# Kernel tuning notes

Measured on AMD Instinct MI355X. Metric: run time of the kernel, lower is better.

## Reference

```python
import jax, jax.numpy as jnp
import numpy as np

N_HEADS = 4
NUM_GROUPS = 32
EPS = 1e-6


def _nin(t, W, b):
    # 1x1 conv as dense over channel dim: [B,C,H,W] x [C,D] -> [B,D,H,W]
    return jnp.einsum('bchw,cd->bdhw', t, W) + b[None, :, None, None]


def setup_inputs() -> dict:
    key = jax.random.key(0)
    ks = jax.random.split(key, 12)
    B, C, H, W = 8, 256, 32, 32
    Tc = 512
    Cin = C + Tc  # 768
    x = jax.random.normal(ks[0], (B, C, H, W), dtype=jnp.float32)
    text_feat = jax.random.normal(ks[1], (B, Tc), dtype=jnp.float32)
    gn_gamma = jnp.ones((Cin,), dtype=jnp.float32)
    gn_beta = jnp.zeros((Cin,), dtype=jnp.float32)
    scale = 1.0 / np.sqrt(Cin)
    W0 = jax.random.normal(ks[2], (Cin, C), dtype=jnp.float32) * scale
    b0 = jnp.zeros((C,), dtype=jnp.float32)
    W1 = jax.random.normal(ks[3], (Cin, C), dtype=jnp.float32) * scale
    b1 = jnp.zeros((C,), dtype=jnp.float32)
    W2 = jax.random.normal(ks[4], (Cin, C), dtype=jnp.float32) * scale
    b2 = jnp.zeros((C,), dtype=jnp.float32)
    return {"x": x, "text_feat": text_feat, "gn_gamma": gn_gamma, "gn_beta": gn_beta,
            "W0": W0, "b0": b0, "W1": W1, "b1": b1, "W2": W2, "b2": b2}


def reference(x, text_feat, gn_gamma, gn_beta, W0, b0, W1, b1, W2, b2):
    B, C, H, W = x.shape
    # broadcast text features spatially and concat on channel dim
    tf = jnp.broadcast_to(text_feat[:, :, None, None], (B, text_feat.shape[1], H, W))
    h = jnp.concatenate([x, tf], axis=1)  # [B, C+Tc, H, W]
    Ctot = h.shape[1]
    # GroupNorm(32, Ctot), eps=1e-6
    hg = h.reshape(B, NUM_GROUPS, Ctot // NUM_GROUPS, H, W)
    mu = hg.mean(axis=(2, 3, 4), keepdims=True)
    var = hg.var(axis=(2, 3, 4), keepdims=True)
    hn = ((hg - mu) * jax.lax.rsqrt(var + EPS)).reshape(B, Ctot, H, W)
    hn = hn * gn_gamma[None, :, None, None] + gn_beta[None, :, None, None]
    q = _nin(hn, W0, b0)
    k = _nin(hn, W1, b1)
    v = _nin(hn, W2, b2)
    Ch = C // N_HEADS
    qh = q.reshape(B * N_HEADS, Ch, H, W)
    kh = k.reshape(B * N_HEADS, Ch, H, W)
    vh = v.reshape(B * N_HEADS, Ch, H, W)
    # full HW x HW attention scores, softmax over flattened key positions
    w = jnp.einsum('bchw,bcij->bhwij', qh, kh) * (Ch ** -0.5)
    w = jax.nn.softmax(w.reshape(B * N_HEADS, H, W, H * W), axis=-1)
    w = w.reshape(B * N_HEADS, H, W, H, W)
    ho = jnp.einsum('bhwij,bcij->bchw', w, vh).reshape(B, C, H, W)
    return x + ho
```

## Files before the change

### kernel.cpp

```cpp
#include <hip/hip_runtime.h>
#include <math.h>

#define BATCH 8
#define CX 256
#define TC 512
#define CIN 768
#define HW_TOT 1024
#define NH 4
#define CHD 64

typedef __attribute__((ext_vector_type(8))) short short8;
typedef __attribute__((ext_vector_type(4))) short s4v;
typedef __attribute__((ext_vector_type(4))) float floatx4;
typedef __attribute__((ext_vector_type(4))) int int4v;

#define QSCALE 0.18033688f

static __device__ __forceinline__ short f2bf(float f) {
    union { float f; unsigned u; } c; c.f = f;
    unsigned r = (c.u + 0x7fffu + ((c.u >> 16) & 1u)) >> 16;
    return (short)r;
}

static __device__ __forceinline__ int pack_trunc(float lo, float hi) {
    union { float f; unsigned u; } L, H;
    L.f = lo; H.f = hi;
    return (int)((H.u & 0xffff0000u) | (L.u >> 16));
}

__global__ __launch_bounds__(256)
void gn_kernel(const float* __restrict__ x, const float* __restrict__ tf,
               const float* __restrict__ gamma, const float* __restrict__ beta,
               float* __restrict__ scale, float* __restrict__ shift,
               float* __restrict__ tc) {
    const int b = blockIdx.x >> 5;
    const int g = blockIdx.x & 31;
    const int t = threadIdx.x;
    const int w = t >> 6, lane = t & 63;
    if (blockIdx.x < 24) tc[blockIdx.x * 256 + t] = 0.f;

    float s = 0.f, ss = 0.f;
    #pragma unroll
    for (int rr = 0; rr < 6; rr++) {
        const int row = w * 6 + rr;
        const int cg = g * 24 + row;
        if (cg < CX) {
            const float4* p = (const float4*)(x + ((size_t)b * CX + cg) * HW_TOT);
            #pragma unroll
            for (int i = 0; i < 4; i++) {
                float4 v = p[lane + 64 * i];
                s += v.x + v.y + v.z + v.w;
                ss += v.x * v.x + v.y * v.y + v.z * v.z + v.w * v.w;
            }
        } else {
            float v = tf[b * TC + cg - CX];
            s += 16.f * v;
            ss += 16.f * v * v;
        }
    }
    #pragma unroll
    for (int d = 1; d < 64; d <<= 1) {
        s += __shfl_xor(s, d);
        ss += __shfl_xor(ss, d);
    }
    __shared__ float rs_[4], rss_[4];
    if (lane == 0) { rs_[w] = s; rss_[w] = ss; }
    __syncthreads();
    const float S  = rs_[0] + rs_[1] + rs_[2] + rs_[3];
    const float SS = rss_[0] + rss_[1] + rss_[2] + rss_[3];
    const float inv_n = 1.f / (24 * 1024);
    const float mean = S * inv_n;
    const float var = SS * inv_n - mean * mean;
    const float r = rsqrtf(var + 1e-6f);
    if (t < 24) {
        int cg = g * 24 + t;
        float sc = gamma[cg] * r;
        scale[b * CIN + cg] = sc;
        shift[b * CIN + cg] = beta[cg] - mean * sc;
    }
}

__global__ __launch_bounds__(256)
void prep_kernel(const float* __restrict__ x, const float* __restrict__ tf,
                 const float* __restrict__ scale, const float* __restrict__ shift,
                 const float* __restrict__ W0, const float* __restrict__ W1,
                 const float* __restrict__ W2,
                 short* __restrict__ hnT, short* __restrict__ Wt,
                 float* __restrict__ tc) {
    __shared__ float hs[128];
    __shared__ float red[4][64];
    const int bx = blockIdx.x;
    const int t = threadIdx.x;
    if (bx < 256) {
        int id = (bx & 31) * 256 + t;
        int b = id >> 10;
        const float* xb = x + (size_t)b * CX * HW_TOT + (id & 1023);
        const float* scb = scale + b * CIN;
        const float* shb = shift + b * CIN;
        short* outp = hnT + (size_t)id * CX;
        int c0base = (bx >> 5) * 32;
        for (int c0 = c0base; c0 < c0base + 32; c0 += 8) {
            short8 o;
            #pragma unroll
            for (int i = 0; i < 8; i++) {
                float v = xb[(size_t)(c0 + i) * HW_TOT];
                o[i] = f2bf(v * scb[c0 + i] + shb[c0 + i]);
            }
            *(short8*)(outp + c0) = o;
        }
    } else if (bx < 268) {
        int m = bx - 256;
        int dg = (m % 3) * 256 + t;
        int which = dg >> 8, d = dg & 255;
        const float* Wm = (which == 0) ? W0 : (which == 1) ? W1 : W2;
        int c0base = (m / 3) * 64;
        for (int c0 = c0base; c0 < c0base + 64; c0 += 8) {
            short8 o;
            #pragma unroll
            for (int i = 0; i < 8; i++) o[i] = f2bf(Wm[(size_t)(c0 + i) * CX + d]);
            *(short8*)(Wt + (size_t)dg * CX + c0) = o;
        }
    } else {
        int m = bx - 268;
        int ks = m & 3;
        int b = (m >> 2) & 7, dt = m >> 5;
        int which = dt >> 2, d0 = (dt & 3) * 64;
        const float* Wm = (which == 0) ? W0 : (which == 1) ? W1 : W2;
        if (t < 128) {
            int c = ks * 128 + t;
            hs[t] = tf[b * TC + c] * scale[b * CIN + CX + c] + shift[b * CIN + CX + c];
        }
        __syncthreads();
        int td = t & 63, tq = t >> 6;
        float acc = 0.f;
        const float* wp = Wm + (size_t)(CX + ks * 128 + tq * 32) * CX + d0 + td;
        #pragma unroll 8
        for (int c = 0; c < 32; c++)
            acc = fmaf(hs[tq * 32 + c], wp[(size_t)c * CX], acc);
        red[tq][td] = acc;
        __syncthreads();
        if (t < 64)
            atomicAdd(&tc[b * CIN + which * CX + d0 + t],
                      red[0][t] + red[1][t] + red[2][t] + red[3][t]);
    }
}

__global__ __launch_bounds__(256, 2)
void qkv_gemm(const short* __restrict__ hnT, const short* __restrict__ Wt,
              const float* __restrict__ tc,
              const float* __restrict__ b0, const float* __restrict__ b1,
              const float* __restrict__ b2,
              short* __restrict__ qb, short* __restrict__ kb, short* __restrict__ vb) {
    const int hw0 = blockIdx.x * 64, dt = blockIdx.y, b = blockIdx.z;
    const int which = dt >> 2;
    const int col0 = (dt & 3) * 64;
    const int dg0 = which * 256 + col0;
    const bool OV = (which == 2);

    __shared__ short At[64 * 256];
    __shared__ short Bt[64 * 256];

    const int t = threadIdx.x;
    const int w = t >> 6, l = t & 63;
    const int wm = w >> 1, wn = w & 1;
    const int l15 = l & 15, q = l >> 4;
    const int srow = t >> 2;
    const int cbase = (t & 3) * 8;
    const int sw = srow & 7;

    const short* gA = hnT + (size_t)(b * HW_TOT + hw0 + srow) * CX + cbase * 8;
    const short* gB = Wt + (size_t)(dg0 + srow) * CX + cbase * 8;

    short8 ra[8], rb[8];
    #pragma unroll
    for (int i = 0; i < 8; i++) ra[i] = *(const short8*)(gA + i * 8);
    #pragma unroll
    for (int i = 0; i < 8; i++) rb[i] = *(const short8*)(gB + i * 8);
    short* wA = At + srow * 256;
    short* wB = Bt + srow * 256;
    #pragma unroll
    for (int i = 0; i < 8; i++) *(short8*)(wA + ((cbase + i) ^ sw) * 8) = ra[i];
    #pragma unroll
    for (int i = 0; i < 8; i++) *(short8*)(wB + ((cbase + i) ^ sw) * 8) = rb[i];
    __syncthreads();

    const short* aB = OV ? Bt : At;
    const short* bB = OV ? At : Bt;

    floatx4 acc[2][2] = {};
    __builtin_amdgcn_s_setprio(1);
    #pragma unroll
    for (int kc = 0; kc < 8; kc++) {
        short8 af[2], bf2[2];
        #pragma unroll
        for (int mt = 0; mt < 2; mt++) {
            const int r = wm * 32 + mt * 16 + l15;
            af[mt] = *(const short8*)(aB + r * 256 + ((kc * 4 + q) ^ (r & 7)) * 8);
        }
        #pragma unroll
        for (int nt = 0; nt < 2; nt++) {
            const int r = wn * 32 + nt * 16 + l15;
            bf2[nt] = *(const short8*)(bB + r * 256 + ((kc * 4 + q) ^ (r & 7)) * 8);
        }
        #pragma unroll
        for (int mt = 0; mt < 2; mt++)
            #pragma unroll
            for (int nt = 0; nt < 2; nt++)
                acc[mt][nt] = __builtin_amdgcn_mfma_f32_16x16x32_bf16(
                    af[mt], bf2[nt], acc[mt][nt], 0, 0, 0);
    }
    __builtin_amdgcn_s_setprio(0);

    __syncthreads();
    const float* bias = (which == 0) ? b0 : (which == 1) ? b1 : b2;
    if (!OV) {
        const float qs = (which == 0) ? QSCALE : 1.0f;
        float cadd[2];
        #pragma unroll
        for (int nt = 0; nt < 2; nt++) {
            int d = col0 + wn * 32 + nt * 16 + l15;
            cadd[nt] = bias[d] + tc[b * CIN + which * CX + d];
        }
        #pragma unroll
        for (int mt = 0; mt < 2; mt++)
            #pragma unroll
            for (int rr = 0; rr < 4; rr++)
                #pragma unroll
                for (int nt = 0; nt < 2; nt++)
                    At[(wm * 32 + mt * 16 + q * 4 + rr) * 72 + wn * 32 + nt * 16 + l15]
                        = f2bf((acc[mt][nt][rr] + cadd[nt]) * qs);
    } else {
        #pragma unroll
        for (int mt = 0; mt < 2; mt++)
            #pragma unroll
            for (int rr = 0; rr < 4; rr++) {
                int d = col0 + wm * 32 + mt * 16 + q * 4 + rr;
                float radd = bias[d] + tc[b * CIN + 2 * CX + d];
                #pragma unroll
                for (int nt = 0; nt < 2; nt++)
                    At[(wm * 32 + mt * 16 + q * 4 + rr) * 72 + wn * 32 + nt * 16 + l15]
                        = f2bf(acc[mt][nt][rr] + radd);
            }
    }
    __syncthreads();
    const int sch2 = (t & 3) * 16;
    short8 v0 = *(const short8*)(At + srow * 72 + sch2);
    short8 v1 = *(const short8*)(At + srow * 72 + sch2 + 8);
    if (!OV) {
        short* outp = (which == 0) ? qb : kb;
        size_t off = (size_t)(b * HW_TOT + hw0 + srow) * CX + col0 + sch2;
        *(short8*)(outp + off) = v0;
        *(short8*)(outp + off + 8) = v1;
    } else {
        size_t off = (size_t)(b * CX + col0 + srow) * HW_TOT + hw0 + sch2;
        *(short8*)(vb + off) = v0;
        *(short8*)(vb + off + 8) = v1;
    }
}

__global__ __launch_bounds__(256, 3)
void attn_kernel(const short* __restrict__ qb, const short* __restrict__ kb,
                 const short* __restrict__ vb, const float* __restrict__ x,
                 float* __restrict__ out) {
    const int qt = blockIdx.x, bh = blockIdx.y;
    const int b = bh >> 2, h = bh & 3;
    const int hw0 = qt * 64;

    __shared__ short Qs[64 * 72];
    __shared__ short Ks[2][64 * 72];
    __shared__ short Vs[2][64 * 72];

    const int t = threadIdx.x;
    const int w = t >> 6, l = t & 63;
    const int pair = w >> 1, jh = w & 1;
    const int l15 = l & 15, q = l >> 4;
    const int srow = t >> 2, sch = (t & 3) * 16;
    const int vpos0 = ((sch >> 5) << 5) + ((sch >> 4) & 1) * 4;

    {
        const short* gq = qb + (size_t)(b * HW_TOT + hw0 + srow) * CX + h * CHD + sch;
        *(short8*)(Qs + srow * 72 + sch)     = *(const short8*)gq;
        *(short8*)(Qs + srow * 72 + sch + 8) = *(const short8*)(gq + 8);
    }

    short8 pk[2][2], pv[2][2];
    #pragma unroll
    for (int s = 0; s < 2; s++) {
        const int j0 = s * 512;
        const short* gk = kb + (size_t)(b * HW_TOT + j0 + srow) * CX + h * CHD + sch;
        pk[s][0] = *(const short8*)gk;
        pk[s][1] = *(const short8*)(gk + 8);
        const short* gv = vb + (size_t)(b * CX + h * CHD + srow) * HW_TOT + j0 + sch;
        pv[s][0] = *(const short8*)gv;
        pv[s][1] = *(const short8*)(gv + 8);
    }
    #pragma unroll
    for (int s = 0; s < 2; s++) {
        *(short8*)(Ks[s] + srow * 72 + sch)     = pk[s][0];
        *(short8*)(Ks[s] + srow * 72 + sch + 8) = pk[s][1];
        short* vrow = Vs[s] + srow * 72 + vpos0;
        *(s4v*)(vrow)      = __builtin_shufflevector(pv[s][0], pv[s][0], 0, 1, 2, 3);
        *(s4v*)(vrow + 8)  = __builtin_shufflevector(pv[s][0], pv[s][0], 4, 5, 6, 7);
        *(s4v*)(vrow + 16) = __builtin_shufflevector(pv[s][1], pv[s][1], 0, 1, 2, 3);
        *(s4v*)(vrow + 24) = __builtin_shufflevector(pv[s][1], pv[s][1], 4, 5, 6, 7);
    }
    __syncthreads();

    short8 aq[2][2];
    #pragma unroll
    for (int g = 0; g < 2; g++) {
        aq[g][0] = *(const short8*)(Qs + (pair * 32 + g * 16 + l15) * 72 + q * 8);
        aq[g][1] = *(const short8*)(Qs + (pair * 32 + g * 16 + l15) * 72 + 32 + q * 8);
    }

    union { int4v i; short8 s; } ones;
    ones.i[0] = 0x3f803f80; ones.i[1] = 0x3f803f80;
    ones.i[2] = 0x3f803f80; ones.i[3] = 0x3f803f80;

    floatx4 oacc[2][4] = {};
    floatx4 lacc[2] = {};
    const short* Kc = Ks[jh];
    const short* Vc = Vs[jh];

    for (int jj = 0; jj < 8; jj++) {
        if (jj < 7) {
            #pragma unroll
            for (int s = 0; s < 2; s++) {
                const int j0 = s * 512 + (jj + 1) * 64;
                const short* gk = kb + (size_t)(b * HW_TOT + j0 + srow) * CX + h * CHD + sch;
                pk[s][0] = *(const short8*)gk;
                pk[s][1] = *(const short8*)(gk + 8);
                const short* gv = vb + (size_t)(b * CX + h * CHD + srow) * HW_TOT + j0 + sch;
                pv[s][0] = *(const short8*)gv;
                pv[s][1] = *(const short8*)(gv + 8);
            }
        }

        floatx4 sacc[2][4] = {};
        __builtin_amdgcn_s_setprio(1);
        #pragma unroll
        for (int nt = 0; nt < 4; nt++) {
            short8 kf0 = *(const short8*)(Kc + (nt * 16 + l15) * 72 + q * 8);
            short8 kf1 = *(const short8*)(Kc + (nt * 16 + l15) * 72 + 32 + q * 8);
            #pragma unroll
            for (int g = 0; g < 2; g++) {
                sacc[g][nt] = __builtin_amdgcn_mfma_f32_16x16x32_bf16(kf0, aq[g][0], sacc[g][nt], 0, 0, 0);
                sacc[g][nt] = __builtin_amdgcn_mfma_f32_16x16x32_bf16(kf1, aq[g][1], sacc[g][nt], 0, 0, 0);
            }
        }
        __builtin_amdgcn_s_setprio(0);

        union { int4v i; short8 s; } u[2][2];
        #pragma unroll
        for (int g = 0; g < 2; g++)
            #pragma unroll
            for (int nt = 0; nt < 4; nt++) {
                float e0 = exp2f(sacc[g][nt][0]);
                float e1 = exp2f(sacc[g][nt][1]);
                float e2 = exp2f(sacc[g][nt][2]);
                float e3 = exp2f(sacc[g][nt][3]);
                u[g][nt >> 1].i[(nt & 1) * 2]     = pack_trunc(e0, e1);
                u[g][nt >> 1].i[(nt & 1) * 2 + 1] = pack_trunc(e2, e3);
            }

        __builtin_amdgcn_s_setprio(1);
        #pragma unroll
        for (int g = 0; g < 2; g++) {
            lacc[g] = __builtin_amdgcn_mfma_f32_16x16x32_bf16(ones.s, u[g][0].s, lacc[g], 0, 0, 0);
            lacc[g] = __builtin_amdgcn_mfma_f32_16x16x32_bf16(ones.s, u[g][1].s, lacc[g], 0, 0, 0);
        }

        #pragma unroll
        for (int ct = 0; ct < 4; ct++) {
            const short* vr = Vc + (ct * 16 + l15) * 72;
            #pragma unroll
            for (int kcc = 0; kcc < 2; kcc++) {
                short8 vf = *(const short8*)(vr + kcc * 32 + q * 8);
                #pragma unroll
                for (int g = 0; g < 2; g++)
                    oacc[g][ct] = __builtin_amdgcn_mfma_f32_16x16x32_bf16(
                        vf, u[g][kcc].s, oacc[g][ct], 0, 0, 0);
            }
        }
        __builtin_amdgcn_s_setprio(0);

        if (jj < 7) {
            __syncthreads();
            #pragma unroll
            for (int s = 0; s < 2; s++) {
                *(short8*)(Ks[s] + srow * 72 + sch)     = pk[s][0];
                *(short8*)(Ks[s] + srow * 72 + sch + 8) = pk[s][1];
                short* vrow = Vs[s] + srow * 72 + vpos0;
                *(s4v*)(vrow)      = __builtin_shufflevector(pv[s][0], pv[s][0], 0, 1, 2, 3);
                *(s4v*)(vrow + 8)  = __builtin_shufflevector(pv[s][0], pv[s][0], 4, 5, 6, 7);
                *(s4v*)(vrow + 16) = __builtin_shufflevector(pv[s][1], pv[s][1], 0, 1, 2, 3);
                *(s4v*)(vrow + 24) = __builtin_shufflevector(pv[s][1], pv[s][1], 4, 5, 6, 7);
            }
            __syncthreads();
        }
    }

    __syncthreads();
    float* Of = (float*)Ks;
    float* Lf = (float*)Vs;
    if (jh == 1) {
        #pragma unroll
        for (int g = 0; g < 2; g++) {
            int qi = pair * 32 + g * 16 + l15;
            #pragma unroll
            for (int ct = 0; ct < 4; ct++)
                *(floatx4*)&Of[qi * 68 + ct * 16 + q * 4] = oacc[g][ct];
            if (q == 0) Lf[qi] = lacc[g][0];
        }
    }
    __syncthreads();
    if (jh == 0) {
        #pragma unroll
        for (int g = 0; g < 2; g++) {
            int qi = pair * 32 + g * 16 + l15;
            const float rinv = 1.f / (lacc[g][0] + Lf[qi]);
            #pragma unroll
            for (int ct = 0; ct < 4; ct++) {
                floatx4 po = *(const floatx4*)&Of[qi * 68 + ct * 16 + q * 4];
                #pragma unroll
                for (int r = 0; r < 4; r++) {
                    int c = h * CHD + ct * 16 + q * 4 + r;
                    size_t idx = (size_t)(b * CX + c) * HW_TOT + hw0 + qi;
                    out[idx] = x[idx] + (oacc[g][ct][r] + po[r]) * rinv;
                }
            }
        }
    }
}

extern "C" void kernel_launch(void* const* d_in, const int* in_sizes, int n_in,
                              void* d_out, int out_size, void* d_ws, size_t ws_size,
                              hipStream_t stream) {
    (void)in_sizes; (void)n_in; (void)out_size; (void)ws_size;
    const float* x     = (const float*)d_in[0];
    const float* tf    = (const float*)d_in[1];
    const float* gamma = (const float*)d_in[2];
    const float* beta  = (const float*)d_in[3];
    const float* W0 = (const float*)d_in[4];
    const float* b0 = (const float*)d_in[5];
    const float* W1 = (const float*)d_in[6];
    const float* b1 = (const float*)d_in[7];
    const float* W2 = (const float*)d_in[8];
    const float* b2 = (const float*)d_in[9];

    char* ws = (char*)d_ws;
    float* scale  = (float*)(ws);
    float* shift  = (float*)(ws + 24576);
    float* tcb    = (float*)(ws + 49152);
    short* Wt     = (short*)(ws + 73728);
    short* hnT    = (short*)(ws + 466944);
    short* qb     = (short*)(ws + 4661248);
    short* kb     = (short*)(ws + 8855552);
    short* vb     = (short*)(ws + 13049856);

    hipLaunchKernelGGL(gn_kernel, dim3(256), dim3(256), 0, stream,
                       x, tf, gamma, beta, scale, shift, tcb);
    hipLaunchKernelGGL(prep_kernel, dim3(652), dim3(256), 0, stream,
                       x, tf, scale, shift, W0, W1, W2, hnT, Wt, tcb);
    hipLaunchKernelGGL(qkv_gemm, dim3(16, 12, BATCH), dim3(256), 0, stream,
                       hnT, Wt, tcb, b0, b1, b2, qb, kb, vb);
    hipLaunchKernelGGL(attn_kernel, dim3(16, 32), dim3(256), 0, stream,
                       qb, kb, vb, x, (float*)d_out);
}
```

Before: 123.1 us.

## Fuse all four stages into one cooperative persistent kernel with grid syncs

Replaces the four separate launches (groupnorm stats, prep/transpose, QKV GEMM, attention) with a single cooperative persistent kernel that loops over work units per phase and separates phases with grid.sync(). The goal is to remove launch gaps and inter-kernel drain/fill overhead. The QKV GEMM inside the fused kernel is restructured to stream K in 64-wide chunks through a smaller padded LDS tile, because the fused kernel uses a 32 KB shared buffer and targets two blocks per CU. Grid-wide barriers and the tighter LDS budget may cost more than the launch overhead saved. The old multi-kernel path is kept as a fallback if the cooperative launch fails.

Result: slower. 237.9 us (+93.3%).

```diff
diff --git a/kernel.cpp b/kernel.cpp
--- a/kernel.cpp
+++ b/kernel.cpp
@@ -1,5 +1,8 @@
 #include <hip/hip_runtime.h>
+#include <hip/hip_cooperative_groups.h>
 #include <math.h>
+
+namespace cg = cooperative_groups;
 
 #define BATCH 8
 #define CX 256
@@ -26,6 +29,403 @@
     union { float f; unsigned u; } L, H;
     L.f = lo; H.f = hi;
     return (int)((H.u & 0xffff0000u) | (L.u >> 16));
+}
+
+__global__ __launch_bounds__(256, 2)
+void fused_kernel(const float* __restrict__ x, const float* __restrict__ tf,
+                  const float* __restrict__ gamma, const float* __restrict__ beta,
+                  const float* __restrict__ W0, const float* __restrict__ b0,
+                  const float* __restrict__ W1, const float* __restrict__ b1,
+                  const float* __restrict__ W2, const float* __restrict__ b2,
+                  float* __restrict__ scale, float* __restrict__ shift,
+                  float* __restrict__ tc, short* __restrict__ Wt,
+                  short* __restrict__ hnT, short* __restrict__ qb,
+                  short* __restrict__ kb, short* __restrict__ vb,
+                  float* __restrict__ out)
+{
+    __shared__ __align__(16) short SMs[16384];
+    cg::grid_group grid = cg::this_grid();
+    const int bx = blockIdx.x;
+    const int gdx = gridDim.x;
+    const int t = threadIdx.x;
+    const int w = t >> 6, l = t & 63;
+    const int l15 = l & 15, q = l >> 4;
+    const int srow = t >> 2, sch = (t & 3) * 16;
+
+    for (int u = bx; u < 268; u += gdx) {
+        __syncthreads();
+        if (u < 256) {
+            const int b = u >> 5;
+            const int g = u & 31;
+            if (u < 24) tc[u * 256 + t] = 0.f;
+
+            float s = 0.f, ss = 0.f;
+            #pragma unroll
+            for (int rr = 0; rr < 6; rr++) {
+                const int row = w * 6 + rr;
+                const int cg_ = g * 24 + row;
+                if (cg_ < CX) {
+                    const float4* p = (const float4*)(x + ((size_t)b * CX + cg_) * HW_TOT);
+                    #pragma unroll
+                    for (int i = 0; i < 4; i++) {
+                        float4 v = p[l + 64 * i];
+                        s += v.x + v.y + v.z + v.w;
+                        ss += v.x * v.x + v.y * v.y + v.z * v.z + v.w * v.w;
+                    }
+                } else {
+                    float v = tf[b * TC + cg_ - CX];
+                    s += 16.f * v;
+                    ss += 16.f * v * v;
+                }
+            }
+            #pragma unroll
+            for (int d = 1; d < 64; d <<= 1) {
+                s += __shfl_xor(s, d);
+                ss += __shfl_xor(ss, d);
+            }
+            float* rs_ = (float*)SMs;
+            float* rss_ = rs_ + 4;
+            if (l == 0) { rs_[w] = s; rss_[w] = ss; }
+            __syncthreads();
+            const float S  = rs_[0] + rs_[1] + rs_[2] + rs_[3];
+            const float SS = rss_[0] + rss_[1] + rss_[2] + rss_[3];
+            const float inv_n = 1.f / (24 * 1024);
+            const float mean = S * inv_n;
+            const float var = SS * inv_n - mean * mean;
+            const float r = rsqrtf(var + 1e-6f);
+            if (t < 24) {
+                int cg_ = g * 24 + t;
+                float sc = gamma[cg_] * r;
+                scale[b * CIN + cg_] = sc;
+                shift[b * CIN + cg_] = beta[cg_] - mean * sc;
+            }
+        } else {
+            int m = u - 256;
+            int dg = (m % 3) * 256 + t;
+            int which = dg >> 8, d = dg & 255;
+            const float* Wm = (which == 0) ? W0 : (which == 1) ? W1 : W2;
+            int c0base = (m / 3) * 64;
+            for (int c0 = c0base; c0 < c0base + 64; c0 += 8) {
+                short8 o;
+                #pragma unroll
+                for (int i = 0; i < 8; i++) o[i] = f2bf(Wm[(size_t)(c0 + i) * CX + d]);
+                *(short8*)(Wt + (size_t)dg * CX + c0) = o;
+            }
+        }
+    }
+    grid.sync();
+
+    for (int u = bx; u < 640; u += gdx) {
+        __syncthreads();
+        if (u < 256) {
+            int id = (u & 31) * 256 + t;
+            int b = id >> 10;
+            const float* xb = x + (size_t)b * CX * HW_TOT + (id & 1023);
+            const float* scb = scale + b * CIN;
+            const float* shb = shift + b * CIN;
+            short* outp = hnT + (size_t)id * CX;
+            int c0base = (u >> 5) * 32;
+            for (int c0 = c0base; c0 < c0base + 32; c0 += 8) {
+                short8 o;
+                #pragma unroll
+                for (int i = 0; i < 8; i++) {
+                    float v = xb[(size_t)(c0 + i) * HW_TOT];
+                    o[i] = f2bf(v * scb[c0 + i] + shb[c0 + i]);
+                }
+                *(short8*)(outp + c0) = o;
+            }
+        } else {
+            float* hs = (float*)SMs;
+            float (*red)[64] = (float(*)[64])(hs + 128);
+            int m = u - 256;
+            int ks = m & 3;
+            int b = (m >> 2) & 7, dt = m >> 5;
+            int which = dt >> 2, d0 = (dt & 3) * 64;
+            const float* Wm = (which == 0) ? W0 : (which == 1) ? W1 : W2;
+            if (t < 128) {
+                int c = ks * 128 + t;
+                hs[t] = tf[b * TC + c] * scale[b * CIN + CX + c] + shift[b * CIN + CX + c];
+            }
+            __syncthreads();
+            int td = t & 63, tq = t >> 6;
+            float acc = 0.f;
+            const float* wp = Wm + (size_t)(CX + ks * 128 + tq * 32) * CX + d0 + td;
+            #pragma unroll 8
+            for (int c = 0; c < 32; c++)
+                acc = fmaf(hs[tq * 32 + c], wp[(size_t)c * CX], acc);
+            red[tq][td] = acc;
+            __syncthreads();
+            if (t < 64)
+                atomicAdd(&tc[b * CIN + which * CX + d0 + t],
+                          red[0][t] + red[1][t] + red[2][t] + red[3][t]);
+        }
+    }
+    grid.sync();
+
+    {
+        short* At = SMs;
+        short* Bt = SMs + 4608;
+        const int wm = w >> 1, wn = w & 1;
+
+        for (int u = bx; u < 1536; u += gdx) {
+            __syncthreads();
+            const int b = u / 192;
+            const int rem = u - b * 192;
+            const int dt = rem >> 4;
+            const int hw0 = (rem & 15) * 64;
+            const int which = dt >> 2;
+            const int col0 = (dt & 3) * 64;
+            const int dg0 = which * 256 + col0;
+            const bool OV = (which == 2);
+
+            const short* gA = hnT + (size_t)(b * HW_TOT + hw0 + srow) * CX + sch;
+            const short* gB = Wt + (size_t)(dg0 + srow) * CX + sch;
+
+            floatx4 acc[2][2] = {};
+            for (int k0 = 0; k0 < CX; k0 += 64) {
+                __syncthreads();
+                *(short8*)(At + srow * 72 + sch)     = *(const short8*)(gA + k0);
+                *(short8*)(At + srow * 72 + sch + 8) = *(const short8*)(gA + k0 + 8);
+                *(short8*)(Bt + srow * 72 + sch)     = *(const short8*)(gB + k0);
+                *(short8*)(Bt + srow * 72 + sch + 8) = *(const short8*)(gB + k0 + 8);
+                __syncthreads();
+                const short* aB = OV ? Bt : At;
+                const short* bB = OV ? At : Bt;
+                #pragma unroll
+                for (int kc = 0; kc < 2; kc++) {
+                    short8 af[2], bf2[2];
+                    #pragma unroll
+                    for (int mt = 0; mt < 2; mt++)
+                        af[mt] = *(const short8*)(aB + (wm * 32 + mt * 16 + l15) * 72 + kc * 32 + q * 8);
+                    #pragma unroll
+                    for (int nt = 0; nt < 2; nt++)
+                        bf2[nt] = *(const short8*)(bB + (wn * 32 + nt * 16 + l15) * 72 + kc * 32 + q * 8);
+                    #pragma unroll
+                    for (int mt = 0; mt < 2; mt++)
+                        #pragma unroll
+                        for (int nt = 0; nt < 2; nt++)
+                            acc[mt][nt] = __builtin_amdgcn_mfma_f32_16x16x32_bf16(
+                                af[mt], bf2[nt], acc[mt][nt], 0, 0, 0);
+                }
+            }
+
+            __syncthreads();
+            const float* bias = (which == 0) ? b0 : (which == 1) ? b1 : b2;
+            if (!OV) {
+                const float qs = (which == 0) ? QSCALE : 1.0f;
+                float cadd[2];
+                #pragma unroll
+                for (int nt = 0; nt < 2; nt++) {
+                    int d = col0 + wn * 32 + nt * 16 + l15;
+                    cadd[nt] = bias[d] + tc[b * CIN + which * CX + d];
+                }
+                #pragma unroll
+                for (int mt = 0; mt < 2; mt++)
+                    #pragma unroll
+                    for (int rr = 0; rr < 4; rr++)
+                        #pragma unroll
+                        for (int nt = 0; nt < 2; nt++)
+                            At[(wm * 32 + mt * 16 + q * 4 + rr) * 72 + wn * 32 + nt * 16 + l15]
+                                = f2bf((acc[mt][nt][rr] + cadd[nt]) * qs);
+            } else {
+                #pragma unroll
+                for (int mt = 0; mt < 2; mt++)
+                    #pragma unroll
+                    for (int rr = 0; rr < 4; rr++) {
+                        int d = col0 + wm * 32 + mt * 16 + q * 4 + rr;
+                        float radd = bias[d] + tc[b * CIN + 2 * CX + d];
+                        #pragma unroll
+                        for (int nt = 0; nt < 2; nt++)
+                            At[(wm * 32 + mt * 16 + q * 4 + rr) * 72 + wn * 32 + nt * 16 + l15]
+                                = f2bf(acc[mt][nt][rr] + radd);
+                    }
+            }
+            __syncthreads();
+            short8 v0 = *(const short8*)(At + srow * 72 + sch);
+            short8 v1 = *(const short8*)(At + srow * 72 + sch + 8);
+            if (!OV) {
+                short* outp = (which == 0) ? qb : kb;
+                size_t off = (size_t)(b * HW_TOT + hw0 + srow) * CX + col0 + sch;
+                *(short8*)(outp + off) = v0;
+                *(short8*)(outp + off + 8) = v1;
+            } else {
+                size_t off = (size_t)(b * CX + col0 + srow) * HW_TOT + hw0 + sch;
+                *(short8*)(vb + off) = v0;
+                *(short8*)(vb + off + 8) = v1;
+            }
+        }
+    }
+    grid.sync();
+
+    {
+        const int pair = w >> 1, jh = w & 1;
+        const int sw7 = srow & 7;
+        const int kc0 = (t & 3) * 2;
+        const int vpos0 = ((sch >> 5) << 5) + ((sch >> 4) & 1) * 4;
+        const int vc0 = vpos0 >> 3;
+        const int voff = vpos0 & 7;
+
+        union { int4v i; short8 s; } ones;
+        ones.i[0] = 0x3f803f80; ones.i[1] = 0x3f803f80;
+        ones.i[2] = 0x3f803f80; ones.i[3] = 0x3f803f80;
+
+        for (int u = bx; u < 512; u += gdx) {
+            __syncthreads();
+            const int qt = u & 15, bh = u >> 4;
+            const int b = bh >> 2, h = bh & 3;
+            const int hw0 = qt * 64;
+
+            short8 aq[2][2];
+            #pragma unroll
+            for (int g = 0; g < 2; g++) {
+                const short* gq = qb + (size_t)(b * HW_TOT + hw0 + pair * 32 + g * 16 + l15) * CX
+                                  + h * CHD + q * 8;
+                aq[g][0] = *(const short8*)gq;
+                aq[g][1] = *(const short8*)(gq + 32);
+            }
+
+            short8 pk[2][2], pv[2][2];
+            #pragma unroll
+            for (int s = 0; s < 2; s++) {
+                const int j0 = s * 512;
+                const short* gk = kb + (size_t)(b * HW_TOT + j0 + srow) * CX + h * CHD + sch;
+                pk[s][0] = *(const short8*)gk;
+                pk[s][1] = *(const short8*)(gk + 8);
+                const short* gv = vb + (size_t)(b * CX + h * CHD + srow) * HW_TOT + j0 + sch;
+                pv[s][0] = *(const short8*)gv;
+                pv[s][1] = *(const short8*)(gv + 8);
+            }
+            #pragma unroll
+            for (int s = 0; s < 2; s++) {
+                short* Ksp = SMs + s * 4096 + srow * 64;
+                short* Vsp = SMs + 8192 + s * 4096 + srow * 64;
+                *(short8*)(Ksp + ((kc0    ) ^ sw7) * 8) = pk[s][0];
+                *(short8*)(Ksp + ((kc0 + 1) ^ sw7) * 8) = pk[s][1];
+                *(s4v*)(Vsp + ((vc0    ) ^ sw7) * 8 + voff) = __builtin_shufflevector(pv[s][0], pv[s][0], 0, 1, 2, 3);
+                *(s4v*)(Vsp + ((vc0 + 1) ^ sw7) * 8 + voff) = __builtin_shufflevector(pv[s][0], pv[s][0], 4, 5, 6, 7);
+                *(s4v*)(Vsp + ((vc0 + 2) ^ sw7) * 8 + voff) = __builtin_shufflevector(pv[s][1], pv[s][1], 0, 1, 2, 3);
+                *(s4v*)(Vsp + ((vc0 + 3) ^ sw7) * 8 + voff) = __builtin_shufflevector(pv[s][1], pv[s][1], 4, 5, 6, 7);
+            }
+            __syncthreads();
+
+            floatx4 oacc[2][4] = {};
+            floatx4 lacc[2] = {};
+            const short* Kc = SMs + jh * 4096;
+            const short* Vc = SMs + 8192 + jh * 4096;
+
+            for (int jj = 0; jj < 8; jj++) {
+                if (jj < 7) {
+                    #pragma unroll
+                    for (int s = 0; s < 2; s++) {
+                        const int j0 = s * 512 + (jj + 1) * 64;
+                        const short* gk = kb + (size_t)(b * HW_TOT + j0 + srow) * CX + h * CHD + sch;
+                        pk[s][0] = *(const short8*)gk;
+                        pk[s][1] = *(const short8*)(gk + 8);
+                        const short* gv = vb + (size_t)(b * CX + h * CHD + srow) * HW_TOT + j0 + sch;
+                        pv[s][0] = *(const short8*)gv;
+                        pv[s][1] = *(const short8*)(gv + 8);
+                    }
+                }
+
+                floatx4 sacc[2][4] = {};
+                __builtin_amdgcn_s_setprio(1);
+                #pragma unroll
+                for (int nt = 0; nt < 4; nt++) {
+                    const int r = nt * 16 + l15;
+                    short8 kf0 = *(const short8*)(Kc + r * 64 + ((q    ) ^ (r & 7)) * 8);
+                    short8 kf1 = *(const short8*)(Kc + r * 64 + ((4 + q) ^ (r & 7)) * 8);
+                    #pragma unroll
+                    for (int g = 0; g < 2; g++) {
+                        sacc[g][nt] = __builtin_amdgcn_mfma_f32_16x16x32_bf16(kf0, aq[g][0], sacc[g][nt], 0, 0, 0);
+                        sacc[g][nt] = __builtin_amdgcn_mfma_f32_16x16x32_bf16(kf1, aq[g][1], sacc[g][nt], 0, 0, 0);
+                    }
+                }
+                __builtin_amdgcn_s_setprio(0);
+
+                union { int4v i; short8 s; } uu[2][2];
+                #pragma unroll
+                for (int g = 0; g < 2; g++)
+                    #pragma unroll
+                    for (int nt = 0; nt < 4; nt++) {
+                        float e0 = exp2f(sacc[g][nt][0]);
+                        float e1 = exp2f(sacc[g][nt][1]);
+                        float e2 = exp2f(sacc[g][nt][2]);
+                        float e3 = exp2f(sacc[g][nt][3]);
+                        uu[g][nt >> 1].i[(nt & 1) * 2]     = pack_trunc(e0, e1);
+                        uu[g][nt >> 1].i[(nt & 1) * 2 + 1] = pack_trunc(e2, e3);
+                    }
+
+                __builtin_amdgcn_s_setprio(1);
+                #pragma unroll
+                for (int g = 0; g < 2; g++) {
+                    lacc[g] = __builtin_amdgcn_mfma_f32_16x16x32_bf16(ones.s, uu[g][0].s, lacc[g], 0, 0, 0);
+                    lacc[g] = __builtin_amdgcn_mfma_f32_16x16x32_bf16(ones.s, uu[g][1].s, lacc[g], 0, 0, 0);
+                }
+
+                #pragma unroll
+                for (int ct = 0; ct < 4; ct++) {
+                    const int rv = ct * 16 + l15;
+                    #pragma unroll
+                    for (int kcc = 0; kcc < 2; kcc++) {
+                        short8 vf = *(const short8*)(Vc + rv * 64 + ((kcc * 4 + q) ^ (rv & 7)) * 8);
+                        #pragma unroll
+                        for (int g = 0; g < 2; g++)
+                            oacc[g][ct] = __builtin_amdgcn_mfma_f32_16x16x32_bf16(
+                                vf, uu[g][kcc].s, oacc[g][ct], 0, 0, 0);
+                    }
+                }
+                __builtin_amdgcn_s_setprio(0);
+
+                if (jj < 7) {
+                    __syncthreads();
+                    #pragma unroll
+                    for (int s = 0; s < 2; s++) {
+                        short* Ksp = SMs + s * 4096 + srow * 64;
+                        short* Vsp = SMs + 8192 + s * 4096 + srow * 64;
+                        *(short8*)(Ksp + ((kc0    ) ^ sw7) * 8) = pk[s][0];
+                        *(short8*)(Ksp + ((kc0 + 1) ^ sw7) * 8) = pk[s][1];
+                        *(s4v*)(Vsp + ((vc0    ) ^ sw7) * 8 + voff) = __builtin_shufflevector(pv[s][0], pv[s][0], 0, 1, 2, 3);
+                        *(s4v*)(Vsp + ((vc0 + 1) ^ sw7) * 8 + voff) = __builtin_shufflevector(pv[s][0], pv[s][0], 4, 5, 6, 7);
+                        *(s4v*)(Vsp + ((vc0 + 2) ^ sw7) * 8 + voff) = __builtin_shufflevector(pv[s][1], pv[s][1], 0, 1, 2, 3);
+                        *(s4v*)(Vsp + ((vc0 + 3) ^ sw7) * 8 + voff) = __builtin_shufflevector(pv[s][1], pv[s][1], 4, 5, 6, 7);
+                    }
+                    __syncthreads();
+                }
+            }
+
+            __syncthreads();
+            float* Of = (float*)SMs;
+            float* Lf = ((float*)SMs) + 64 * 68;
+            if (jh == 1) {
+                #pragma unroll
+                for (int g = 0; g < 2; g++) {
+                    int qi = pair * 32 + g * 16 + l15;
+                    #pragma unroll
+                    for (int ct = 0; ct < 4; ct++)
+                        *(floatx4*)&Of[qi * 68 + ct * 16 + q * 4] = oacc[g][ct];
+                    if (q == 0) Lf[qi] = lacc[g][0];
+                }
+            }
+            __syncthreads();
+            if (jh == 0) {
+                #pragma unroll
+                for (int g = 0; g < 2; g++) {
+                    int qi = pair * 32 + g * 16 + l15;
+                    const float rinv = 1.f / (lacc[g][0] + Lf[qi]);
+                    #pragma unroll
+                    for (int ct = 0; ct < 4; ct++) {
+                        floatx4 po = *(const floatx4*)&Of[qi * 68 + ct * 16 + q * 4];
+                        #pragma unroll
+                        for (int r = 0; r < 4; r++) {
+                            int c = h * CHD + ct * 16 + q * 4 + r;
+                            size_t idx = (size_t)(b * CX + c) * HW_TOT + hw0 + qi;
+                            out[idx] = x[idx] + (oacc[g][ct][r] + po[r]) * rinv;
+                        }
+                    }
+                }
+            }
+        }
+    }
 }
 
 __global__ __launch_bounds__(256)
@@ -194,13 +594,13 @@
         short8 af[2], bf2[2];
         #pragma unroll
         for (int mt = 0; mt < 2; mt++) {
-            const int r = wm * 32 + mt * 16 + l15;
-            af[mt] = *(const short8*)(aB + r * 256 + ((kc * 4 + q) ^ (r & 7)) * 8);
+            const int rr = wm * 32 + mt * 16 + l15;
+            af[mt] = *(const short8*)(aB + rr * 256 + ((kc * 4 + q) ^ (rr & 7)) * 8);
         }
         #pragma unroll
         for (int nt = 0; nt < 2; nt++) {
-            const int r = wn * 32 + nt * 16 + l15;
-            bf2[nt] = *(const short8*)(bB + r * 256 + ((kc * 4 + q) ^ (r & 7)) * 8);
+            const int rr = wn * 32 + nt * 16 + l15;
+            bf2[nt] = *(const short8*)(bB + rr * 256 + ((kc * 4 + q) ^ (rr & 7)) * 8);
         }
         #pragma unroll
         for (int mt = 0; mt < 2; mt++)
@@ -457,13 +857,30 @@
     short* qb     = (short*)(ws + 4661248);
     short* kb     = (short*)(ws + 8855552);
     short* vb     = (short*)(ws + 13049856);
-
-    hipLaunchKernelGGL(gn_kernel, dim3(256), dim3(256), 0, stream,
-                       x, tf, gamma, beta, scale, shift, tcb);
-    hipLaunchKernelGGL(prep_kernel, dim3(652), dim3(256), 0, stream,
-                       x, tf, scale, shift, W0, W1, W2, hnT, Wt, tcb);
-    hipLaunchKernelGGL(qkv_gemm, dim3(16, 12, BATCH), dim3(256), 0, stream,
-                       hnT, Wt, tcb, b0, b1, b2, qb, kb, vb);
-    hipLaunchKernelGGL(attn_kernel, dim3(16, 32), dim3(256), 0, stream,
-                       qb, kb, vb, x, (float*)d_out);
+    float* outp   = (float*)d_out;
+
+    int mb = 0;
+    hipError_t qe = hipOccupancyMaxActiveBlocksPerMultiprocessor(&mb, fused_kernel, 256, 0);
+    hipError_t le = hipErrorUnknown;
+    if (qe == hipSuccess && mb >= 1) {
+        int gridN = (mb >= 2) ? 512 : 256;
+        void* args[] = { (void*)&x, (void*)&tf, (void*)&gamma, (void*)&beta,
+                         (void*)&W0, (void*)&b0, (void*)&W1, (void*)&b1,
+                         (void*)&W2, (void*)&b2,
+                         (void*)&scale, (void*)&shift, (void*)&tcb, (void*)&Wt,
+                         (void*)&hnT, (void*)&qb, (void*)&kb, (void*)&vb,
+                         (void*)&outp };
+        le = hipLaunchCooperativeKernel((const void*)fused_kernel, dim3(gridN),
+                                        dim3(256), args, 0, stream);
+    }
+    if (le != hipSuccess) {
+        hipLaunchKernelGGL(gn_kernel, dim3(256), dim3(256), 0, stream,
+                           x, tf, gamma, beta, scale, shift, tcb);
+        hipLaunchKernelGGL(prep_kernel, dim3(652), dim3(256), 0, stream,
+                           x, tf, scale, shift, W0, W1, W2, hnT, Wt, tcb);
+        hipLaunchKernelGGL(qkv_gemm, dim3(16, 12, BATCH), dim3(256), 0, stream,
+                           hnT, Wt, tcb, b0, b1, b2, qb, kb, vb);
+        hipLaunchKernelGGL(attn_kernel, dim3(16, 32), dim3(256), 0, stream,
+                           qb, kb, vb, x, outp);
+    }
 }
```

## Split attention keys across four waves per query pair with swizzled LDS

Applied to the files above, without the earlier changes.

The attention kernel now runs 512 threads per block: each pair of waves becomes four waves that each handle a quarter of the key range. Half the threads stage K and the other half stage V into an XOR-swizzled unpadded LDS layout, which shortens the loop from 8 to 4 iterations. Q fragments are loaded straight from global memory into registers instead of going through LDS. Partial outputs are combined through LDS in three serialized reduction steps. The group-norm kernel also moves to 512 threads with fewer rows per wave. More waves per block raise occupancy and latency hiding, at the cost of extra reduction syncs and larger LDS use (64KB).

New measurement: 138.2 us. +12.3%, slower.

```diff
diff --git a/kernel.cpp b/kernel.cpp
--- a/kernel.cpp
+++ b/kernel.cpp
@@ -28,7 +28,7 @@
     return (int)((H.u & 0xffff0000u) | (L.u >> 16));
 }
 
-__global__ __launch_bounds__(256)
+__global__ __launch_bounds__(512)
 void gn_kernel(const float* __restrict__ x, const float* __restrict__ tf,
                const float* __restrict__ gamma, const float* __restrict__ beta,
                float* __restrict__ scale, float* __restrict__ shift,
@@ -37,12 +37,12 @@
     const int g = blockIdx.x & 31;
     const int t = threadIdx.x;
     const int w = t >> 6, lane = t & 63;
-    if (blockIdx.x < 24) tc[blockIdx.x * 256 + t] = 0.f;
+    if (blockIdx.x < 12) tc[blockIdx.x * 512 + t] = 0.f;
 
     float s = 0.f, ss = 0.f;
     #pragma unroll
-    for (int rr = 0; rr < 6; rr++) {
-        const int row = w * 6 + rr;
+    for (int rr = 0; rr < 3; rr++) {
+        const int row = w * 3 + rr;
         const int cg = g * 24 + row;
         if (cg < CX) {
             const float4* p = (const float4*)(x + ((size_t)b * CX + cg) * HW_TOT);
@@ -63,11 +63,12 @@
         s += __shfl_xor(s, d);
         ss += __shfl_xor(ss, d);
     }
-    __shared__ float rs_[4], rss_[4];
+    __shared__ float rs_[8], rss_[8];
     if (lane == 0) { rs_[w] = s; rss_[w] = ss; }
     __syncthreads();
-    const float S  = rs_[0] + rs_[1] + rs_[2] + rs_[3];
-    const float SS = rss_[0] + rss_[1] + rss_[2] + rss_[3];
+    float S = 0.f, SS = 0.f;
+    #pragma unroll
+    for (int i = 0; i < 8; i++) { S += rs_[i]; SS += rss_[i]; }
     const float inv_n = 1.f / (24 * 1024);
     const float mean = S * inv_n;
     const float var = SS * inv_n - mean * mean;
@@ -194,13 +195,13 @@
         short8 af[2], bf2[2];
         #pragma unroll
         for (int mt = 0; mt < 2; mt++) {
-            const int r = wm * 32 + mt * 16 + l15;
-            af[mt] = *(const short8*)(aB + r * 256 + ((kc * 4 + q) ^ (r & 7)) * 8);
+            const int rr = wm * 32 + mt * 16 + l15;
+            af[mt] = *(const short8*)(aB + rr * 256 + ((kc * 4 + q) ^ (rr & 7)) * 8);
         }
         #pragma unroll
         for (int nt = 0; nt < 2; nt++) {
-            const int r = wn * 32 + nt * 16 + l15;
-            bf2[nt] = *(const short8*)(bB + r * 256 + ((kc * 4 + q) ^ (r & 7)) * 8);
+            const int rr = wn * 32 + nt * 16 + l15;
+            bf2[nt] = *(const short8*)(bB + rr * 256 + ((kc * 4 + q) ^ (rr & 7)) * 8);
         }
         #pragma unroll
         for (int mt = 0; mt < 2; mt++)
@@ -258,60 +259,69 @@
     }
 }
 
-__global__ __launch_bounds__(256, 3)
+__global__ __launch_bounds__(512, 4)
 void attn_kernel(const short* __restrict__ qb, const short* __restrict__ kb,
                  const short* __restrict__ vb, const float* __restrict__ x,
                  float* __restrict__ out) {
+    __shared__ __align__(16) short SMs[32768];
+
     const int qt = blockIdx.x, bh = blockIdx.y;
     const int b = bh >> 2, h = bh & 3;
     const int hw0 = qt * 64;
 
-    __shared__ short Qs[64 * 72];
-    __shared__ short Ks[2][64 * 72];
-    __shared__ short Vs[2][64 * 72];
-
     const int t = threadIdx.x;
     const int w = t >> 6, l = t & 63;
-    const int pair = w >> 1, jh = w & 1;
+    const int pair = w >> 2;
+    const int jq = w & 3;
     const int l15 = l & 15, q = l >> 4;
-    const int srow = t >> 2, sch = (t & 3) * 16;
+    const int t256 = t & 255;
+    const int srow = t256 >> 2, sch = (t256 & 3) * 16;
+    const int sw7 = srow & 7;
+    const int kc0 = (t256 & 3) * 2;
     const int vpos0 = ((sch >> 5) << 5) + ((sch >> 4) & 1) * 4;
-
-    {
-        const short* gq = qb + (size_t)(b * HW_TOT + hw0 + srow) * CX + h * CHD + sch;
-        *(short8*)(Qs + srow * 72 + sch)     = *(const short8*)gq;
-        *(short8*)(Qs + srow * 72 + sch + 8) = *(const short8*)(gq + 8);
-    }
-
-    short8 pk[2][2], pv[2][2];
-    #pragma unroll
-    for (int s = 0; s < 2; s++) {
-        const int j0 = s * 512;
-        const short* gk = kb + (size_t)(b * HW_TOT + j0 + srow) * CX + h * CHD + sch;
-        pk[s][0] = *(const short8*)gk;
-        pk[s][1] = *(const short8*)(gk + 8);
-        const short* gv = vb + (size_t)(b * CX + h * CHD + srow) * HW_TOT + j0 + sch;
-        pv[s][0] = *(const short8*)gv;
-        pv[s][1] = *(const short8*)(gv + 8);
-    }
-    #pragma unroll
-    for (int s = 0; s < 2; s++) {
-        *(short8*)(Ks[s] + srow * 72 + sch)     = pk[s][0];
-        *(short8*)(Ks[s] + srow * 72 + sch + 8) = pk[s][1];
-        short* vrow = Vs[s] + srow * 72 + vpos0;
-        *(s4v*)(vrow)      = __builtin_shufflevector(pv[s][0], pv[s][0], 0, 1, 2, 3);
-        *(s4v*)(vrow + 8)  = __builtin_shufflevector(pv[s][0], pv[s][0], 4, 5, 6, 7);
-        *(s4v*)(vrow + 16) = __builtin_shufflevector(pv[s][1], pv[s][1], 0, 1, 2, 3);
-        *(s4v*)(vrow + 24) = __builtin_shufflevector(pv[s][1], pv[s][1], 4, 5, 6, 7);
-    }
-    __syncthreads();
+    const int vc0 = vpos0 >> 3, voff = vpos0 & 7;
+    const bool grpA = (t < 256);
 
     short8 aq[2][2];
     #pragma unroll
     for (int g = 0; g < 2; g++) {
-        aq[g][0] = *(const short8*)(Qs + (pair * 32 + g * 16 + l15) * 72 + q * 8);
-        aq[g][1] = *(const short8*)(Qs + (pair * 32 + g * 16 + l15) * 72 + 32 + q * 8);
-    }
+        const short* gq = qb + (size_t)(b * HW_TOT + hw0 + pair * 32 + g * 16 + l15) * CX
+                          + h * CHD + q * 8;
+        aq[g][0] = *(const short8*)gq;
+        aq[g][1] = *(const short8*)(gq + 32);
+    }
+
+    short8 pf[4][2];
+    if (grpA) {
+        #pragma unroll
+        for (int s = 0; s < 4; s++) {
+            const short* gk = kb + (size_t)(b * HW_TOT + s * 256 + srow) * CX + h * CHD + sch;
+            pf[s][0] = *(const short8*)gk;
+            pf[s][1] = *(const short8*)(gk + 8);
+        }
+        #pragma unroll
+        for (int s = 0; s < 4; s++) {
+            short* Ksp = SMs + s * 4096 + srow * 64;
+            *(short8*)(Ksp + ((kc0    ) ^ sw7) * 8) = pf[s][0];
+            *(short8*)(Ksp + ((kc0 + 1) ^ sw7) * 8) = pf[s][1];
+        }
+    } else {
+        #pragma unroll
+        for (int s = 0; s < 4; s++) {
+            const short* gv = vb + (size_t)(b * CX + h * CHD + srow) * HW_TOT + s * 256 + sch;
+            pf[s][0] = *(const short8*)gv;
+            pf[s][1] = *(const short8*)(gv + 8);
+        }
+        #pragma unroll
+        for (int s = 0; s < 4; s++) {
+            short* Vsp = SMs + 16384 + s * 4096 + srow * 64;
+            *(s4v*)(Vsp + ((vc0    ) ^ sw7) * 8 + voff) = __builtin_shufflevector(pf[s][0], pf[s][0], 0, 1, 2, 3);
+            *(s4v*)(Vsp + ((vc0 + 1) ^ sw7) * 8 + voff) = __builtin_shufflevector(pf[s][0], pf[s][0], 4, 5, 6, 7);
+            *(s4v*)(Vsp + ((vc0 + 2) ^ sw7) * 8 + voff) = __builtin_shufflevector(pf[s][1], pf[s][1], 0, 1, 2, 3);
+            *(s4v*)(Vsp + ((vc0 + 3) ^ sw7) * 8 + voff) = __builtin_shufflevector(pf[s][1], pf[s][1], 4, 5, 6, 7);
+        }
+    }
+    __syncthreads();
 
     union { int4v i; short8 s; } ones;
     ones.i[0] = 0x3f803f80; ones.i[1] = 0x3f803f80;
@@ -319,20 +329,25 @@
 
     floatx4 oacc[2][4] = {};
     floatx4 lacc[2] = {};
-    const short* Kc = Ks[jh];
-    const short* Vc = Vs[jh];
-
-    for (int jj = 0; jj < 8; jj++) {
-        if (jj < 7) {
-            #pragma unroll
-            for (int s = 0; s < 2; s++) {
-                const int j0 = s * 512 + (jj + 1) * 64;
-                const short* gk = kb + (size_t)(b * HW_TOT + j0 + srow) * CX + h * CHD + sch;
-                pk[s][0] = *(const short8*)gk;
-                pk[s][1] = *(const short8*)(gk + 8);
-                const short* gv = vb + (size_t)(b * CX + h * CHD + srow) * HW_TOT + j0 + sch;
-                pv[s][0] = *(const short8*)gv;
-                pv[s][1] = *(const short8*)(gv + 8);
+    const short* Kc = SMs + jq * 4096;
+    const short* Vc = SMs + 16384 + jq * 4096;
+
+    for (int jj = 0; jj < 4; jj++) {
+        if (jj < 3) {
+            if (grpA) {
+                #pragma unroll
+                for (int s = 0; s < 4; s++) {
+                    const short* gk = kb + (size_t)(b * HW_TOT + s * 256 + (jj + 1) * 64 + srow) * CX + h * CHD + sch;
+                    pf[s][0] = *(const short8*)gk;
+                    pf[s][1] = *(const short8*)(gk + 8);
+                }
+            } else {
+                #pragma unroll
+                for (int s = 0; s < 4; s++) {
+                    const short* gv = vb + (size_t)(b * CX + h * CHD + srow) * HW_TOT + s * 256 + (jj + 1) * 64 + sch;
+                    pf[s][0] = *(const short8*)gv;
+                    pf[s][1] = *(const short8*)(gv + 8);
+                }
             }
         }
 
@@ -340,8 +355,9 @@
         __builtin_amdgcn_s_setprio(1);
         #pragma unroll
         for (int nt = 0; nt < 4; nt++) {
-            short8 kf0 = *(const short8*)(Kc + (nt * 16 + l15) * 72 + q * 8);
-            short8 kf1 = *(const short8*)(Kc + (nt * 16 + l15) * 72 + 32 + q * 8);
+            const int r = nt * 16 + l15;
+            short8 kf0 = *(const short8*)(Kc + r * 64 + ((q    ) ^ (r & 7)) * 8);
+            short8 kf1 = *(const short8*)(Kc + r * 64 + ((4 + q) ^ (r & 7)) * 8);
             #pragma unroll
             for (int g = 0; g < 2; g++) {
                 sacc[g][nt] = __builtin_amdgcn_mfma_f32_16x16x32_bf16(kf0, aq[g][0], sacc[g][nt], 0, 0, 0);
@@ -350,7 +366,7 @@
         }
         __builtin_amdgcn_s_setprio(0);
 
-        union { int4v i; short8 s; } u[2][2];
+        union { int4v i; short8 s; } uu[2][2];
         #pragma unroll
         for (int g = 0; g < 2; g++)
             #pragma unroll
@@ -359,51 +375,58 @@
                 float e1 = exp2f(sacc[g][nt][1]);
                 float e2 = exp2f(sacc[g][nt][2]);
                 float e3 = exp2f(sacc[g][nt][3]);
-                u[g][nt >> 1].i[(nt & 1) * 2]     = pack_trunc(e0, e1);
-                u[g][nt >> 1].i[(nt & 1) * 2 + 1] = pack_trunc(e2, e3);
+                uu[g][nt >> 1].i[(nt & 1) * 2]     = pack_trunc(e0, e1);
+                uu[g][nt >> 1].i[(nt & 1) * 2 + 1] = pack_trunc(e2, e3);
             }
 
         __builtin_amdgcn_s_setprio(1);
         #pragma unroll
         for (int g = 0; g < 2; g++) {
-            lacc[g] = __builtin_amdgcn_mfma_f32_16x16x32_bf16(ones.s, u[g][0].s, lacc[g], 0, 0, 0);
-            lacc[g] = __builtin_amdgcn_mfma_f32_16x16x32_bf16(ones.s, u[g][1].s, lacc[g], 0, 0, 0);
+            lacc[g] = __builtin_amdgcn_mfma_f32_16x16x32_bf16(ones.s, uu[g][0].s, lacc[g], 0, 0, 0);
+            lacc[g] = __builtin_amdgcn_mfma_f32_16x16x32_bf16(ones.s, uu[g][1].s, lacc[g], 0, 0, 0);
         }
 
         #pragma unroll
         for (int ct = 0; ct < 4; ct++) {
-            const short* vr = Vc + (ct * 16 + l15) * 72;
+            const int rv = ct * 16 + l15;
             #pragma unroll
             for (int kcc = 0; kcc < 2; kcc++) {
-                short8 vf = *(const short8*)(vr + kcc * 32 + q * 8);
+                short8 vf = *(const short8*)(Vc + rv * 64 + ((kcc * 4 + q) ^ (rv & 7)) * 8);
                 #pragma unroll
                 for (int g = 0; g < 2; g++)
                     oacc[g][ct] = __builtin_amdgcn_mfma_f32_16x16x32_bf16(
-                        vf, u[g][kcc].s, oacc[g][ct], 0, 0, 0);
+                        vf, uu[g][kcc].s, oacc[g][ct], 0, 0, 0);
             }
         }
         __builtin_amdgcn_s_setprio(0);
 
-        if (jj < 7) {
+        if (jj < 3) {
             __syncthreads();
-            #pragma unroll
-            for (int s = 0; s < 2; s++) {
-                *(short8*)(Ks[s] + srow * 72 + sch)     = pk[s][0];
-                *(short8*)(Ks[s] + srow * 72 + sch + 8) = pk[s][1];
-                short* vrow = Vs[s] + srow * 72 + vpos0;
-                *(s4v*)(vrow)      = __builtin_shufflevector(pv[s][0], pv[s][0], 0, 1, 2, 3);
-                *(s4v*)(vrow + 8)  = __builtin_shufflevector(pv[s][0], pv[s][0], 4, 5, 6, 7);
-                *(s4v*)(vrow + 16) = __builtin_shufflevector(pv[s][1], pv[s][1], 0, 1, 2, 3);
-                *(s4v*)(vrow + 24) = __builtin_shufflevector(pv[s][1], pv[s][1], 4, 5, 6, 7);
+            if (grpA) {
+                #pragma unroll
+                for (int s = 0; s < 4; s++) {
+                    short* Ksp = SMs + s * 4096 + srow * 64;
+                    *(short8*)(Ksp + ((kc0    ) ^ sw7) * 8) = pf[s][0];
+                    *(short8*)(Ksp + ((kc0 + 1) ^ sw7) * 8) = pf[s][1];
+                }
+            } else {
+                #pragma unroll
+                for (int s = 0; s < 4; s++) {
+                    short* Vsp = SMs + 16384 + s * 4096 + srow * 64;
+                    *(s4v*)(Vsp + ((vc0    ) ^ sw7) * 8 + voff) = __builtin_shufflevector(pf[s][0], pf[s][0], 0, 1, 2, 3);
+                    *(s4v*)(Vsp + ((vc0 + 1) ^ sw7) * 8 + voff) = __builtin_shufflevector(pf[s][0], pf[s][0], 4, 5, 6, 7);
+                    *(s4v*)(Vsp + ((vc0 + 2) ^ sw7) * 8 + voff) = __builtin_shufflevector(pf[s][1], pf[s][1], 0, 1, 2, 3);
+                    *(s4v*)(Vsp + ((vc0 + 3) ^ sw7) * 8 + voff) = __builtin_shufflevector(pf[s][1], pf[s][1], 4, 5, 6, 7);
+                }
             }
             __syncthreads();
         }
     }
 
     __syncthreads();
-    float* Of = (float*)Ks;
-    float* Lf = (float*)Vs;
-    if (jh == 1) {
+    float* Of = (float*)SMs;
+    float* Lf = ((float*)SMs) + 64 * 68;
+    if (jq == 3) {
         #pragma unroll
         for (int g = 0; g < 2; g++) {
             int qi = pair * 32 + g * 16 + l15;
@@ -414,7 +437,33 @@
         }
     }
     __syncthreads();
-    if (jh == 0) {
+    if (jq == 2) {
+        #pragma unroll
+        for (int g = 0; g < 2; g++) {
+            int qi = pair * 32 + g * 16 + l15;
+            #pragma unroll
+            for (int ct = 0; ct < 4; ct++) {
+                floatx4 po = *(const floatx4*)&Of[qi * 68 + ct * 16 + q * 4];
+                *(floatx4*)&Of[qi * 68 + ct * 16 + q * 4] = po + oacc[g][ct];
+            }
+            if (q == 0) Lf[qi] += lacc[g][0];
+        }
+    }
+    __syncthreads();
+    if (jq == 1) {
+        #pragma unroll
+        for (int g = 0; g < 2; g++) {
+            int qi = pair * 32 + g * 16 + l15;
+            #pragma unroll
+            for (int ct = 0; ct < 4; ct++) {
+                floatx4 po = *(const floatx4*)&Of[qi * 68 + ct * 16 + q * 4];
+                *(floatx4*)&Of[qi * 68 + ct * 16 + q * 4] = po + oacc[g][ct];
+            }
+            if (q == 0) Lf[qi] += lacc[g][0];
+        }
+    }
+    __syncthreads();
+    if (jq == 0) {
         #pragma unroll
         for (int g = 0; g < 2; g++) {
             int qi = pair * 32 + g * 16 + l15;
@@ -458,12 +507,12 @@
     short* kb     = (short*)(ws + 8855552);
     short* vb     = (short*)(ws + 13049856);
 
-    hipLaunchKernelGGL(gn_kernel, dim3(256), dim3(256), 0, stream,
+    hipLaunchKernelGGL(gn_kernel, dim3(256), dim3(512), 0, stream,
                        x, tf, gamma, beta, scale, shift, tcb);
     hipLaunchKernelGGL(prep_kernel, dim3(652), dim3(256), 0, stream,
                        x, tf, scale, shift, W0, W1, W2, hnT, Wt, tcb);
     hipLaunchKernelGGL(qkv_gemm, dim3(16, 12, BATCH), dim3(256), 0, stream,
                        hnT, Wt, tcb, b0, b1, b2, qb, kb, vb);
-    hipLaunchKernelGGL(attn_kernel, dim3(16, 32), dim3(256), 0, stream,
+    hipLaunchKernelGGL(attn_kernel, dim3(16, 32), dim3(512), 0, stream,
                        qb, kb, vb, x, (float*)d_out);
 }
```
